# Optimization experiments

Measured on AMD Instinct MI355X. Metric: run time of the kernel, lower is better.

Reference implementation:

```python
import jax, jax.numpy as jnp
import numpy as np

DIM = 1280
NUM_HEADS = 16
HEAD_DIM = DIM // NUM_HEADS  # 80
HIDDEN = DIM * 4             # 5120
SEQ = 4096
EPS = 1e-6


def _layernorm(x, scale, bias):
    mu = jnp.mean(x, axis=-1, keepdims=True)
    var = jnp.mean((x - mu) ** 2, axis=-1, keepdims=True)
    return (x - mu) * jax.lax.rsqrt(var + EPS) * scale + bias


def _rotate_half(x):
    x1, x2 = jnp.split(x, 2, axis=-1)
    return jnp.concatenate([-x2, x1], axis=-1)


def _apply_rope(x, freqs):
    # x: [N, H, D], freqs: [N, D//2]
    orig = x.dtype
    x = x.astype(jnp.float32)
    cos = jnp.repeat(jnp.cos(freqs), 2, axis=-1)[:, None, :].astype(jnp.float32)  # [N,1,D]
    sin = jnp.repeat(jnp.sin(freqs), 2, axis=-1)[:, None, :].astype(jnp.float32)
    return (x * cos + _rotate_half(x) * sin).astype(orig)


def _quick_gelu(x):
    return x * jax.nn.sigmoid(1.702 * x)


def setup_inputs() -> dict:
    key = jax.random.key(0)
    ks = jax.random.split(key, 12)
    s = 0.02
    inp = {
        "hidden_states": jax.random.normal(ks[0], (SEQ, DIM), dtype=jnp.float32),
        "rotary_pos_emb": jax.random.normal(ks[1], (SEQ, HEAD_DIM // 2), dtype=jnp.float32),
        "cu_seqlens": jnp.array([0, 1024, 2048, 3072, 4096], dtype=jnp.int32),
        "w_qkv": jax.random.normal(ks[2], (DIM, 3 * DIM), dtype=jnp.float32) * s,
        "b_qkv": jnp.zeros((3 * DIM,), dtype=jnp.float32),
        "w_proj": jax.random.normal(ks[3], (DIM, DIM), dtype=jnp.float32) * s,
        "b_proj": jnp.zeros((DIM,), dtype=jnp.float32),
        "w_fc1": jax.random.normal(ks[4], (DIM, HIDDEN), dtype=jnp.float32) * s,
        "b_fc1": jnp.zeros((HIDDEN,), dtype=jnp.float32),
        "w_fc2": jax.random.normal(ks[5], (HIDDEN, DIM), dtype=jnp.float32) * s,
        "b_fc2": jnp.zeros((DIM,), dtype=jnp.float32),
        "ln1_scale": jnp.ones((DIM,), dtype=jnp.float32),
        "ln1_bias": jnp.zeros((DIM,), dtype=jnp.float32),
        "ln2_scale": jnp.ones((DIM,), dtype=jnp.float32),
        "ln2_bias": jnp.zeros((DIM,), dtype=jnp.float32),
    }
    return inp


def _attention(x, cu_seqlens, rotary_pos_emb, w_qkv, b_qkv, w_proj, b_proj):
    N = x.shape[0]
    qkv = (x @ w_qkv + b_qkv).reshape(N, 3, NUM_HEADS, HEAD_DIM)
    q, k, v = qkv[:, 0], qkv[:, 1], qkv[:, 2]  # each [N, H, D]
    q = _apply_rope(q, rotary_pos_emb)
    k = _apply_rope(k, rotary_pos_emb)
    # block-diagonal mask from cu_seqlens (faithful to original construction)
    row_ids = jnp.arange(N)[None, None, :]
    col_ids = jnp.arange(N)[None, :, None]
    starts = cu_seqlens[:-1][:, None, None]
    ends = cu_seqlens[1:][:, None, None]
    is_valid = (row_ids >= starts) & (row_ids < ends) & (col_ids >= starts) & (col_ids < ends)
    combined = jnp.any(is_valid, axis=0)  # [N, N]
    bias = jnp.where(combined, 0.0, jnp.finfo(q.dtype).min)
    scores = jnp.einsum("shd,thd->hst", q, k) / np.sqrt(HEAD_DIM).astype(np.float32)
    scores = scores + bias[None, :, :]
    probs = jax.nn.softmax(scores.astype(jnp.float32), axis=-1).astype(q.dtype)
    out = jnp.einsum("hst,thd->shd", probs, v).reshape(N, DIM)
    return out @ w_proj + b_proj


def reference(hidden_states, rotary_pos_emb, cu_seqlens, w_qkv, b_qkv, w_proj, b_proj,
              w_fc1, b_fc1, w_fc2, b_fc2, ln1_scale, ln1_bias, ln2_scale, ln2_bias):
    h = hidden_states
    h = h + _attention(_layernorm(h, ln1_scale, ln1_bias), cu_seqlens, rotary_pos_emb,
                       w_qkv, b_qkv, w_proj, b_proj)
    m = _layernorm(h, ln2_scale, ln2_bias)
    h = h + (_quick_gelu(m @ w_fc1 + b_fc1) @ w_fc2 + b_fc2)
    return h
```

## Files before the change

### kernel.cpp

```cpp
#include <hip/hip_runtime.h>
#include <hip/hip_bf16.h>
#include <math.h>

typedef __bf16 bf16;
typedef __bf16 bf16x8 __attribute__((ext_vector_type(8)));
typedef float f32x4 __attribute__((ext_vector_type(4)));

#define DIM 1280
#define SEQ 4096
#define NH 16
#define HD 80
#define HIDDEN 5120
#define FLAG_THRESH 4096

__device__ __forceinline__ void gl_lds16(const bf16* g, bf16* l) {
  __builtin_amdgcn_global_load_lds((const __attribute__((address_space(1))) void*)g,
                                   (__attribute__((address_space(3))) void*)l, 16, 0, 0);
}

__device__ __forceinline__ f32x4 fz4() { f32x4 v; v.x = 0.f; v.y = 0.f; v.z = 0.f; v.w = 0.f; return v; }

__device__ __forceinline__ float ldx(const void* p, size_t i, bool f32) {
  if (f32) return ((const float*)p)[i];
  return (float)((const bf16*)p)[i];
}

__global__ void zero_flag_k(int* flag) { *flag = 0; }

__global__ __launch_bounds__(256) void sniff_k(const unsigned short* h, int n, int* flag) {
  int i = blockIdx.x * 256 + threadIdx.x;
  int c = 0;
  for (int idx = i; idx < n; idx += 256 * gridDim.x) {
    int e = (h[idx] >> 7) & 0xFF;
    c += (e >= 0xC8) ? 1 : 0;
  }
  #pragma unroll
  for (int o = 32; o; o >>= 1) c += __shfl_down(c, o);
  if ((threadIdx.x & 63) == 0 && c) atomicAdd(flag, c);
}

__global__ __launch_bounds__(256) void transpose_k(const void* __restrict__ in, bf16* __restrict__ out,
                                                   int R, int C, const int* __restrict__ flag) {
  bool f32 = *flag > FLAG_THRESH;
  __shared__ bf16 tile[32][33];
  int c0 = blockIdx.x * 32, r0 = blockIdx.y * 32;
  int tx = threadIdx.x, ty = threadIdx.y;
  #pragma unroll
  for (int i = 0; i < 4; i++)
    tile[ty + 8 * i][tx] = (bf16)ldx(in, (size_t)(r0 + ty + 8 * i) * C + c0 + tx, f32);
  __syncthreads();
  #pragma unroll
  for (int i = 0; i < 4; i++)
    out[(size_t)(c0 + ty + 8 * i) * R + r0 + tx] = tile[tx][ty + 8 * i];
}

__global__ __launch_bounds__(256) void ln_k(const void* __restrict__ x, const void* __restrict__ sc,
                                            const void* __restrict__ bi, bf16* __restrict__ out,
                                            const int* __restrict__ flag, int force_f32) {
  bool pf32 = *flag > FLAG_THRESH;
  bool xf32 = force_f32 || pf32;
  int row = blockIdx.x, t = threadIdx.x;
  float v[5];
  float s = 0.f, sq = 0.f;
  #pragma unroll
  for (int i = 0; i < 5; i++) {
    v[i] = ldx(x, (size_t)row * DIM + i * 256 + t, xf32);
    s += v[i]; sq += v[i] * v[i];
  }
  #pragma unroll
  for (int o = 32; o; o >>= 1) { s += __shfl_down(s, o); sq += __shfl_down(sq, o); }
  __shared__ float rs[4], rq[4];
  if ((t & 63) == 0) { rs[t >> 6] = s; rq[t >> 6] = sq; }
  __syncthreads();
  s = rs[0] + rs[1] + rs[2] + rs[3];
  sq = rq[0] + rq[1] + rq[2] + rq[3];
  float mean = s * (1.f / DIM);
  float var = sq * (1.f / DIM) - mean * mean;
  float rstd = rsqrtf(fmaxf(var, 0.f) + 1e-6f);
  #pragma unroll
  for (int i = 0; i < 5; i++) {
    int c = i * 256 + t;
    out[(size_t)row * DIM + c] = (bf16)((v[i] - mean) * rstd * ldx(sc, c, pf32) + ldx(bi, c, pf32));
  }
}

template <int TN>
__device__ __forceinline__ void gemm_step(const bf16* As, const bf16* Bs, f32x4 (&acc)[4][TN],
                                          int wm, int wn, int quad, int l15) {
  bf16x8 af[4], bfr[TN];
  #pragma unroll
  for (int tm = 0; tm < 4; tm++) af[tm] = *(const bf16x8*)&As[(wm + tm * 16 + l15) * 32 + quad * 8];
  #pragma unroll
  for (int tn = 0; tn < TN; tn++) bfr[tn] = *(const bf16x8*)&Bs[(wn + tn * 16 + l15) * 32 + quad * 8];
  #pragma unroll
  for (int tm = 0; tm < 4; tm++)
    #pragma unroll
    for (int tn = 0; tn < TN; tn++)
      acc[tm][tn] = __builtin_amdgcn_mfma_f32_16x16x32_bf16(af[tm], bfr[tn], acc[tm][tn], 0, 0, 0);
}

template <int MODE, int NT>
__global__ __launch_bounds__(256) void gemm_bt(const bf16* __restrict__ A, const bf16* __restrict__ Bt,
                                               const void* __restrict__ bias, const void* __restrict__ res,
                                               void* __restrict__ out, int M, int N, int K,
                                               const int* __restrict__ flag) {
  bool pf32 = *flag > FLAG_THRESH;
  constexpr int TN = NT / 32;
  __shared__ bf16 As0[128 * 32];
  __shared__ bf16 As1[128 * 32];
  __shared__ bf16 Bs0[NT * 32];
  __shared__ bf16 Bs1[NT * 32];
  int tid = threadIdx.x;
  int lane = tid & 63, wv = tid >> 6;
  int quad = lane >> 4, l15 = lane & 15;
  int nwg = gridDim.x * gridDim.y;
  int bid = blockIdx.y * gridDim.x + blockIdx.x;
  int sbid = (bid & 7) * (nwg >> 3) + (bid >> 3);
  int bx = sbid % gridDim.x, by = sbid / gridDim.x;
  int m0 = by * 128, n0 = bx * NT;
  int wm = (wv & 1) * 64, wn = (wv >> 1) * (NT / 2);
  const bf16* Ag = A + (size_t)m0 * K;
  const bf16* Bg = Bt + (size_t)n0 * K;
  int r0 = tid >> 2, c0 = (tid & 3) * 8;
  int r1 = r0 + 64;
  f32x4 acc[4][TN];
  #pragma unroll
  for (int i = 0; i < 4; i++)
    #pragma unroll
    for (int j = 0; j < TN; j++) acc[i][j] = fz4();

#define STAGE_BT(as, bs, kk) do {                                        \
    gl_lds16(Ag + (size_t)r0 * K + (kk) + c0, &(as)[tid * 8]);           \
    gl_lds16(Ag + (size_t)r1 * K + (kk) + c0, &(as)[(tid + 256) * 8]);   \
    gl_lds16(Bg + (size_t)r0 * K + (kk) + c0, &(bs)[tid * 8]);           \
    if constexpr (NT == 128) gl_lds16(Bg + (size_t)r1 * K + (kk) + c0, &(bs)[(tid + 256) * 8]); \
  } while (0)

  STAGE_BT(As0, Bs0, 0);
  __syncthreads();
  for (int k0 = 0; k0 < K; k0 += 64) {
    STAGE_BT(As1, Bs1, k0 + 32);
    gemm_step<TN>(As0, Bs0, acc, wm, wn, quad, l15);
    __syncthreads();
    if (k0 + 64 < K) STAGE_BT(As0, Bs0, k0 + 64);
    gemm_step<TN>(As1, Bs1, acc, wm, wn, quad, l15);
    __syncthreads();
  }
#undef STAGE_BT

  #pragma unroll
  for (int tm = 0; tm < 4; tm++) {
    #pragma unroll
    for (int tn = 0; tn < TN; tn++) {
      #pragma unroll
      for (int r = 0; r < 4; r++) {
        int row = m0 + wm + tm * 16 + quad * 4 + r;
        int col = n0 + wn + tn * 16 + l15;
        size_t idx = (size_t)row * N + col;
        float vv = acc[tm][tn][r] + ldx(bias, col, pf32);
        if constexpr (MODE == 0) ((bf16*)out)[idx] = (bf16)vv;
        if constexpr (MODE == 1) ((float*)out)[idx] = vv + ldx(res, idx, pf32);
        if constexpr (MODE == 2) ((bf16*)out)[idx] = (bf16)(vv / (1.f + __expf(-1.702f * vv)));
      }
    }
  }
}

__global__ __launch_bounds__(256) void gemm_sk(const bf16* __restrict__ A, const bf16* __restrict__ Bt,
                                               float* __restrict__ part, int M, int N, int K, int chunk) {
  __shared__ bf16 As0[128 * 32];
  __shared__ bf16 As1[128 * 32];
  __shared__ bf16 Bs0[64 * 32];
  __shared__ bf16 Bs1[64 * 32];
  int tid = threadIdx.x;
  int lane = tid & 63, wv = tid >> 6;
  int quad = lane >> 4, l15 = lane & 15;
  int nwg = gridDim.x * gridDim.y;
  int bid = blockIdx.y * gridDim.x + blockIdx.x;
  int sbid = (bid & 7) * (nwg >> 3) + (bid >> 3);
  int bx = sbid % gridDim.x, by = sbid / gridDim.x;
  int m0 = by * 128, n0 = bx * 64;
  int wm = (wv & 1) * 64, wn = (wv >> 1) * 32;
  int kb = blockIdx.z * chunk;
  const bf16* Ag = A + (size_t)m0 * K;
  const bf16* Bg = Bt + (size_t)n0 * K;
  int r0 = tid >> 2, c0 = (tid & 3) * 8;
  int r1 = r0 + 64;
  f32x4 acc[4][2];
  #pragma unroll
  for (int i = 0; i < 4; i++)
    #pragma unroll
    for (int j = 0; j < 2; j++) acc[i][j] = fz4();

#define STAGE_SK(as, bs, kk) do {                                        \
    gl_lds16(Ag + (size_t)r0 * K + (kk) + c0, &(as)[tid * 8]);           \
    gl_lds16(Ag + (size_t)r1 * K + (kk) + c0, &(as)[(tid + 256) * 8]);   \
    gl_lds16(Bg + (size_t)r0 * K + (kk) + c0, &(bs)[tid * 8]);           \
  } while (0)

  STAGE_SK(As0, Bs0, kb);
  __syncthreads();
  for (int k0 = kb; k0 < kb + chunk; k0 += 64) {
    STAGE_SK(As1, Bs1, k0 + 32);
    gemm_step<2>(As0, Bs0, acc, wm, wn, quad, l15);
    __syncthreads();
    if (k0 + 64 < kb + chunk) STAGE_SK(As0, Bs0, k0 + 64);
    gemm_step<2>(As1, Bs1, acc, wm, wn, quad, l15);
    __syncthreads();
  }
#undef STAGE_SK

  float* po = part + (size_t)blockIdx.z * M * N;
  #pragma unroll
  for (int tm = 0; tm < 4; tm++) {
    #pragma unroll
    for (int tn = 0; tn < 2; tn++) {
      #pragma unroll
      for (int r = 0; r < 4; r++) {
        int row = m0 + wm + tm * 16 + quad * 4 + r;
        int col = n0 + wn + tn * 16 + l15;
        po[(size_t)row * N + col] = acc[tm][tn][r];
      }
    }
  }
}

__global__ __launch_bounds__(256) void reduce2_k(const float* __restrict__ p0, const float* __restrict__ p1,
                                                 const void* __restrict__ bias, const float* __restrict__ res,
                                                 float* __restrict__ out, int NCOL,
                                                 const int* __restrict__ flag) {
  bool pf32 = *flag > FLAG_THRESH;
  size_t i = ((size_t)blockIdx.x * 256 + threadIdx.x) * 4;
  int col = (int)(i % NCOL);
  float4 a = *(const float4*)&p0[i];
  float4 b = *(const float4*)&p1[i];
  float4 r = *(const float4*)&res[i];
  float4 o;
  o.x = a.x + b.x + r.x + ldx(bias, col + 0, pf32);
  o.y = a.y + b.y + r.y + ldx(bias, col + 1, pf32);
  o.z = a.z + b.z + r.z + ldx(bias, col + 2, pf32);
  o.w = a.w + b.w + r.w + ldx(bias, col + 3, pf32);
  *(float4*)&out[i] = o;
}

__global__ __launch_bounds__(256) void rope_k(bf16* __restrict__ qkv, const void* __restrict__ rot,
                                              const int* __restrict__ flag) {
  bool pf32 = *flag > FLAG_THRESH;
  int idx = blockIdx.x * 256 + threadIdx.x;
  int d = idx % 40;
  int t = idx / 40;
  int head = t & 15;
  int seq = t >> 4;
  float f1 = ldx(rot, (size_t)seq * 40 + (d >> 1), pf32);
  float f2 = ldx(rot, (size_t)seq * 40 + (d >> 1) + 20, pf32);
  float c1 = cosf(f1), s1 = sinf(f1), c2 = cosf(f2), s2 = sinf(f2);
  const float scq = 0.11180339887498949f;
  size_t base = (size_t)seq * (3 * DIM) + head * HD + d;
  float x1 = (float)qkv[base], x2 = (float)qkv[base + 40];
  qkv[base] = (bf16)((x1 * c1 - x2 * s1) * scq);
  qkv[base + 40] = (bf16)((x2 * c2 + x1 * s2) * scq);
  x1 = (float)qkv[base + DIM]; x2 = (float)qkv[base + DIM + 40];
  qkv[base + DIM] = (bf16)(x1 * c1 - x2 * s1);
  qkv[base + DIM + 40] = (bf16)(x2 * c2 + x1 * s2);
}

__global__ __launch_bounds__(256, 4) void attn_k(const bf16* __restrict__ qkv, const int* __restrict__ cu,
                                                 bf16* __restrict__ out) {
  __shared__ __align__(16) char smem[38144];
  bf16* Qs = (bf16*)smem;
  bf16* Ks = (bf16*)(smem + 13312);
  bf16* Vt = (bf16*)(smem + 26624);
  bf16* Ps = (bf16*)smem;
  int tid = threadIdx.x, lane = tid & 63, wv = tid >> 6;
  int quad = lane >> 4, l15 = lane & 15;
  int qt = blockIdx.x, head = blockIdx.y, seg = blockIdx.z;
  int s0 = cu[seg], s1 = cu[seg + 1];
  int q0 = s0 + qt * 64;
  if (q0 >= s1) return;
  const bf16* qh = qkv + head * HD;
  const bf16* kh = qkv + DIM + head * HD;
  const bf16* vh = qkv + 2 * DIM + head * HD;
  const int RS = 3 * DIM;
  uint4 z4; z4.x = 0; z4.y = 0; z4.z = 0; z4.w = 0;
  for (int i = tid; i < 128; i += 256) {
    int r = i >> 1, c = i & 1;
    *(uint4*)&Qs[r * 104 + 80 + c * 8] = z4;
    *(uint4*)&Ks[r * 104 + 80 + c * 8] = z4;
  }
  for (int i = tid; i < 640; i += 256) {
    int r = i / 10, c = i % 10;
    *(bf16x8*)&Qs[r * 104 + c * 8] = *(const bf16x8*)&qh[(size_t)(q0 + r) * RS + c * 8];
  }
  __syncthreads();
  bf16x8 aq[3];
  #pragma unroll
  for (int ks = 0; ks < 3; ks++)
    aq[ks] = *(const bf16x8*)&Qs[(wv * 16 + l15) * 104 + ks * 32 + quad * 8];

  float m_r[4], l_r[4];
  f32x4 oacc[5];
  #pragma unroll
  for (int r = 0; r < 4; r++) { m_r[r] = -1e30f; l_r[r] = 0.f; }
  #pragma unroll
  for (int nt = 0; nt < 5; nt++) oacc[nt] = fz4();

  for (int kt = s0; kt < s1; kt += 64) {
    __syncthreads();
    for (int i = tid; i < 640; i += 256) {
      int r = i / 10, c = i % 10;
      *(bf16x8*)&Ks[r * 104 + c * 8] = *(const bf16x8*)&kh[(size_t)(kt + r) * RS + c * 8];
    }
    for (int i = tid; i < 640; i += 256) {
      int c = i >> 6, r = i & 63;
      bf16x8 vv = *(const bf16x8*)&vh[(size_t)(kt + r) * RS + c * 8];
      #pragma unroll
      for (int j = 0; j < 8; j++) Vt[(c * 8 + j) * 72 + r] = vv[j];
    }
    __syncthreads();
    f32x4 sacc[4];
    #pragma unroll
    for (int j = 0; j < 4; j++) sacc[j] = fz4();
    #pragma unroll
    for (int ks = 0; ks < 3; ks++) {
      #pragma unroll
      for (int j = 0; j < 4; j++) {
        bf16x8 bk = *(const bf16x8*)&Ks[(j * 16 + l15) * 104 + ks * 32 + quad * 8];
        sacc[j] = __builtin_amdgcn_mfma_f32_16x16x32_bf16(aq[ks], bk, sacc[j], 0, 0, 0);
      }
    }
    #pragma unroll
    for (int r = 0; r < 4; r++) {
      float mx = fmaxf(fmaxf(sacc[0][r], sacc[1][r]), fmaxf(sacc[2][r], sacc[3][r]));
      #pragma unroll
      for (int o = 8; o; o >>= 1) mx = fmaxf(mx, __shfl_xor(mx, o));
      float mnew = fmaxf(m_r[r], mx);
      float alpha = __expf(m_r[r] - mnew);
      float psum = 0.f;
      #pragma unroll
      for (int j = 0; j < 4; j++) {
        float p = __expf(sacc[j][r] - mnew);
        psum += p;
        Ps[wv * 1152 + (quad * 4 + r) * 72 + j * 16 + l15] = (bf16)p;
      }
      #pragma unroll
      for (int o = 8; o; o >>= 1) psum += __shfl_xor(psum, o);
      l_r[r] = l_r[r] * alpha + psum;
      m_r[r] = mnew;
      #pragma unroll
      for (int nt = 0; nt < 5; nt++) oacc[nt][r] *= alpha;
    }
    #pragma unroll
    for (int ks = 0; ks < 2; ks++) {
      bf16x8 ap = *(const bf16x8*)&Ps[wv * 1152 + l15 * 72 + ks * 32 + quad * 8];
      #pragma unroll
      for (int nt = 0; nt < 5; nt++) {
        bf16x8 bv = *(const bf16x8*)&Vt[(nt * 16 + l15) * 72 + ks * 32 + quad * 8];
        oacc[nt] = __builtin_amdgcn_mfma_f32_16x16x32_bf16(ap, bv, oacc[nt], 0, 0, 0);
      }
    }
  }
  #pragma unroll
  for (int nt = 0; nt < 5; nt++) {
    #pragma unroll
    for (int r = 0; r < 4; r++) {
      int row = q0 + wv * 16 + quad * 4 + r;
      int d = nt * 16 + l15;
      out[(size_t)row * DIM + head * HD + d] = (bf16)(oacc[nt][r] / l_r[r]);
    }
  }
}

#define FLAG_OFF 0UL
#define QKVT_OFF 256UL
#define PROJT_OFF 9830656UL
#define FC1T_OFF 13107456UL
#define FC2T_OFF 26214656UL
#define LN_OFF 39321856UL
#define QKV_OFF 49807616UL
#define PART_OFF 49807616UL
#define AO_OFF 81264896UL
#define H1_OFF 91750656UL
#define FC1O_OFF 112722176UL

extern "C" void kernel_launch(void* const* d_in, const int* in_sizes, int n_in,
                              void* d_out, int out_size, void* d_ws, size_t ws_size,
                              hipStream_t stream) {
  const void* hidden = d_in[0];
  const void* rot    = d_in[1];
  const int*  cu     = (const int*)d_in[2];
  const void* w_qkv  = d_in[3];
  const void* b_qkv  = d_in[4];
  const void* w_proj = d_in[5];
  const void* b_proj = d_in[6];
  const void* w_fc1  = d_in[7];
  const void* b_fc1  = d_in[8];
  const void* w_fc2  = d_in[9];
  const void* b_fc2  = d_in[10];
  const void* ln1s   = d_in[11];
  const void* ln1b   = d_in[12];
  const void* ln2s   = d_in[13];
  const void* ln2b   = d_in[14];

  char* ws = (char*)d_ws;
  int* flag   = (int*)(ws + FLAG_OFF);
  bf16* qkvT  = (bf16*)(ws + QKVT_OFF);
  bf16* projT = (bf16*)(ws + PROJT_OFF);
  bf16* fc1T  = (bf16*)(ws + FC1T_OFF);
  bf16* fc2T  = (bf16*)(ws + FC2T_OFF);
  bf16* ln_bf = (bf16*)(ws + LN_OFF);
  bf16* qkv   = (bf16*)(ws + QKV_OFF);
  float* part = (float*)(ws + PART_OFF);
  bf16* ao    = (bf16*)(ws + AO_OFF);
  float* h1   = (float*)(ws + H1_OFF);
  bf16* fc1o  = (bf16*)(ws + FC1O_OFF);

  zero_flag_k<<<1, 1, 0, stream>>>(flag);
  sniff_k<<<256, 256, 0, stream>>>((const unsigned short*)hidden, SEQ * DIM, flag);

  dim3 tb(32, 8);
  transpose_k<<<dim3(120, 40), tb, 0, stream>>>(w_qkv, qkvT, 1280, 3840, flag);
  transpose_k<<<dim3(40, 40), tb, 0, stream>>>(w_proj, projT, 1280, 1280, flag);
  transpose_k<<<dim3(160, 40), tb, 0, stream>>>(w_fc1, fc1T, 1280, 5120, flag);
  transpose_k<<<dim3(40, 160), tb, 0, stream>>>(w_fc2, fc2T, 5120, 1280, flag);

  ln_k<<<SEQ, 256, 0, stream>>>(hidden, ln1s, ln1b, ln_bf, flag, 0);
  gemm_bt<0, 128><<<dim3(30, 32), 256, 0, stream>>>(ln_bf, qkvT, b_qkv, nullptr, qkv, SEQ, 3 * DIM, DIM, flag);
  rope_k<<<10240, 256, 0, stream>>>(qkv, rot, flag);
  attn_k<<<dim3(16, NH, 4), 256, 0, stream>>>(qkv, cu, ao);
  gemm_bt<1, 64><<<dim3(20, 32), 256, 0, stream>>>(ao, projT, b_proj, hidden, h1, SEQ, DIM, DIM, flag);
  ln_k<<<SEQ, 256, 0, stream>>>(h1, ln2s, ln2b, ln_bf, flag, 1);
  gemm_bt<2, 128><<<dim3(40, 32), 256, 0, stream>>>(ln_bf, fc1T, b_fc1, nullptr, fc1o, SEQ, HIDDEN, DIM, flag);
  gemm_sk<<<dim3(20, 32, 2), 256, 0, stream>>>(fc1o, fc2T, part, SEQ, DIM, HIDDEN, HIDDEN / 2);
  reduce2_k<<<SEQ * DIM / 1024, 256, 0, stream>>>(part, part + (size_t)SEQ * DIM, b_fc2, h1,
                                                  (float*)d_out, DIM, flag);
}
```

Measured before the change: 663.9 us.

## Use explicit vmcnt waits with raw barriers in GEMMs, drop block swizzle, add setprio

Replaces __syncthreads in the double-buffered GEMM loops with explicit s_waitcnt vmcnt counts plus raw s_barrier. The next stage's global-to-LDS loads can then stay in flight while the current buffer is consumed, instead of every wave waiting for all outstanding memory ops. It also removes the XCD-style block index swizzle in favor of plain blockIdx mapping, and raises wave priority around the MFMA sections in attention. Risks: the hand-written vmcnt counts must match the number of issued loads exactly or reads become racy, and dropping the swizzle may hurt L2 locality.

```diff
diff --git a/kernel.cpp b/kernel.cpp
--- a/kernel.cpp
+++ b/kernel.cpp
@@ -12,6 +12,9 @@
 #define HD 80
 #define HIDDEN 5120
 #define FLAG_THRESH 4096
+
+#define S_VMCNT(n) asm volatile("s_waitcnt vmcnt(" #n ")" ::: "memory")
+#define S_BAR() __builtin_amdgcn_s_barrier()
 
 __device__ __forceinline__ void gl_lds16(const bf16* g, bf16* l) {
   __builtin_amdgcn_global_load_lds((const __attribute__((address_space(1))) void*)g,
@@ -113,11 +116,7 @@
   int tid = threadIdx.x;
   int lane = tid & 63, wv = tid >> 6;
   int quad = lane >> 4, l15 = lane & 15;
-  int nwg = gridDim.x * gridDim.y;
-  int bid = blockIdx.y * gridDim.x + blockIdx.x;
-  int sbid = (bid & 7) * (nwg >> 3) + (bid >> 3);
-  int bx = sbid % gridDim.x, by = sbid / gridDim.x;
-  int m0 = by * 128, n0 = bx * NT;
+  int m0 = blockIdx.y * 128, n0 = blockIdx.x * NT;
   int wm = (wv & 1) * 64, wn = (wv >> 1) * (NT / 2);
   const bf16* Ag = A + (size_t)m0 * K;
   const bf16* Bg = Bt + (size_t)n0 * K;
@@ -137,14 +136,21 @@
   } while (0)
 
   STAGE_BT(As0, Bs0, 0);
-  __syncthreads();
   for (int k0 = 0; k0 < K; k0 += 64) {
     STAGE_BT(As1, Bs1, k0 + 32);
+    if constexpr (NT == 128) { S_VMCNT(4); } else { S_VMCNT(3); }
+    S_BAR();
     gemm_step<TN>(As0, Bs0, acc, wm, wn, quad, l15);
-    __syncthreads();
-    if (k0 + 64 < K) STAGE_BT(As0, Bs0, k0 + 64);
+    S_BAR();
+    if (k0 + 64 < K) {
+      STAGE_BT(As0, Bs0, k0 + 64);
+      if constexpr (NT == 128) { S_VMCNT(4); } else { S_VMCNT(3); }
+    } else {
+      S_VMCNT(0);
+    }
+    S_BAR();
     gemm_step<TN>(As1, Bs1, acc, wm, wn, quad, l15);
-    __syncthreads();
+    S_BAR();
   }
 #undef STAGE_BT
 
@@ -175,11 +181,7 @@
   int tid = threadIdx.x;
   int lane = tid & 63, wv = tid >> 6;
   int quad = lane >> 4, l15 = lane & 15;
-  int nwg = gridDim.x * gridDim.y;
-  int bid = blockIdx.y * gridDim.x + blockIdx.x;
-  int sbid = (bid & 7) * (nwg >> 3) + (bid >> 3);
-  int bx = sbid % gridDim.x, by = sbid / gridDim.x;
-  int m0 = by * 128, n0 = bx * 64;
+  int m0 = blockIdx.y * 128, n0 = blockIdx.x * 64;
   int wm = (wv & 1) * 64, wn = (wv >> 1) * 32;
   int kb = blockIdx.z * chunk;
   const bf16* Ag = A + (size_t)m0 * K;
@@ -199,14 +201,21 @@
   } while (0)
 
   STAGE_SK(As0, Bs0, kb);
-  __syncthreads();
   for (int k0 = kb; k0 < kb + chunk; k0 += 64) {
     STAGE_SK(As1, Bs1, k0 + 32);
+    S_VMCNT(3);
+    S_BAR();
     gemm_step<2>(As0, Bs0, acc, wm, wn, quad, l15);
-    __syncthreads();
-    if (k0 + 64 < kb + chunk) STAGE_SK(As0, Bs0, k0 + 64);
+    S_BAR();
+    if (k0 + 64 < kb + chunk) {
+      STAGE_SK(As0, Bs0, k0 + 64);
+      S_VMCNT(3);
+    } else {
+      S_VMCNT(0);
+    }
+    S_BAR();
     gemm_step<2>(As1, Bs1, acc, wm, wn, quad, l15);
-    __syncthreads();
+    S_BAR();
   }
 #undef STAGE_SK
 
@@ -320,6 +329,7 @@
     f32x4 sacc[4];
     #pragma unroll
     for (int j = 0; j < 4; j++) sacc[j] = fz4();
+    __builtin_amdgcn_s_setprio(1);
     #pragma unroll
     for (int ks = 0; ks < 3; ks++) {
       #pragma unroll
@@ -328,6 +338,7 @@
         sacc[j] = __builtin_amdgcn_mfma_f32_16x16x32_bf16(aq[ks], bk, sacc[j], 0, 0, 0);
       }
     }
+    __builtin_amdgcn_s_setprio(0);
     #pragma unroll
     for (int r = 0; r < 4; r++) {
       float mx = fmaxf(fmaxf(sacc[0][r], sacc[1][r]), fmaxf(sacc[2][r], sacc[3][r]));
@@ -349,6 +360,7 @@
       #pragma unroll
       for (int nt = 0; nt < 5; nt++) oacc[nt][r] *= alpha;
     }
+    __builtin_amdgcn_s_setprio(1);
     #pragma unroll
     for (int ks = 0; ks < 2; ks++) {
       bf16x8 ap = *(const bf16x8*)&Ps[wv * 1152 + l15 * 72 + ks * 32 + quad * 8];
@@ -358,6 +370,7 @@
         oacc[nt] = __builtin_amdgcn_mfma_f32_16x16x32_bf16(ap, bv, oacc[nt], 0, 0, 0);
       }
     }
+    __builtin_amdgcn_s_setprio(0);
   }
   #pragma unroll
   for (int nt = 0; nt < 5; nt++) {
```

After: 656.5 us. About the same (-1.1%).
